# Performance work log

Measured on AMD Instinct MI355X. Metric: run time of the kernel, lower is better.

The kernel has to match this reference:

```python
import jax, jax.numpy as jnp
import numpy as np

D = 768
HEAD_DIM = 64
NHEADS = D // HEAD_DIM
B, S = 2, 4096


def setup_inputs() -> dict:
    key = jax.random.key(0)
    ks = jax.random.split(key, 9)
    std = 1.0 / np.sqrt(D)
    inp = {"x": jax.random.normal(ks[0], (B, S, D), dtype=jnp.float32)}
    for i, name in enumerate(["Wq", "Wk", "Wv", "Wo"]):
        inp[name + "_w"] = jax.random.uniform(ks[1 + 2 * i], (D, D), dtype=jnp.float32, minval=-std, maxval=std)
        inp[name + "_b"] = jax.random.uniform(ks[2 + 2 * i], (D,), dtype=jnp.float32, minval=-std, maxval=std)
    return inp


def reference(x, Wq_w, Wq_b, Wk_w, Wk_b, Wv_w, Wv_b, Wo_w, Wo_b):
    b, s, d = x.shape
    # nn.Linear: y = x @ W.T + b
    q = x @ Wq_w.T + Wq_b
    k = x @ Wk_w.T + Wk_b
    v = x @ Wv_w.T + Wv_b
    # [B, H, S, hd]
    q = q.reshape(b, s, NHEADS, HEAD_DIM).transpose(0, 2, 1, 3)
    k = k.reshape(b, s, NHEADS, HEAD_DIM).transpose(0, 2, 1, 3)
    v = v.reshape(b, s, NHEADS, HEAD_DIM).transpose(0, 2, 1, 3)
    scale = jnp.sqrt(jnp.asarray(HEAD_DIM, dtype=q.dtype))
    logits = jnp.einsum('bhqd,bhkd->bhqk', q, k) / scale  # [B,H,S,S]
    causal_mask = jnp.triu(jnp.ones((s, s), dtype=bool), k=1)
    logits = jnp.where(causal_mask, -jnp.inf, logits)
    a = jax.nn.softmax(logits, axis=-1)
    preout = jnp.einsum('bhqk,bhkd->bhqd', a, v)
    preout = preout.transpose(0, 2, 1, 3).reshape(b, s, d)
    return preout @ Wo_w.T + Wo_b
```

## Files before the change

### kernel.cpp

```cpp
#include <hip/hip_runtime.h>

typedef unsigned short u16;
typedef unsigned int u32;
typedef __bf16 bf16_t;
typedef bf16_t bf16x8 __attribute__((ext_vector_type(8)));
typedef float f32x2 __attribute__((ext_vector_type(2)));
typedef float f32x4 __attribute__((ext_vector_type(4)));
typedef float f32x16 __attribute__((ext_vector_type(16)));

#define DM 768
#define HD 64
#define NH 12
#define NB 2
#define SEQ 4096
#define MR (NB * SEQ)

#define SCL2E_F (0.125f * 1.44269504088896340736f)

__device__ __forceinline__ u16 f2bf(float f) {
  union { float f; u32 u; } v;
  v.f = f;
  u32 r = v.u + 0x7FFFu + ((v.u >> 16) & 1u);
  return (u16)(r >> 16);
}

__device__ __forceinline__ u32 cvtpk(float a, float b) {
  u32 r;
  asm("v_cvt_pk_bf16_f32 %0, %1, %2" : "=v"(r) : "v"(a), "v"(b));
  return r;
}

__device__ __forceinline__ void pl32swap(u32& a, u32& b) {
  asm volatile("v_permlane32_swap_b32 %0, %1" : "+v"(a), "+v"(b));
}

__device__ __forceinline__ f32x2 pkadd(f32x2 a, f32x2 b) {
  f32x2 r;
  asm("v_pk_add_f32 %0, %1, %2" : "=v"(r) : "v"(a), "v"(b));
  return r;
}

__device__ __forceinline__ bf16x8 ldb8(const u16* p) {
  return *reinterpret_cast<const bf16x8*>(p);
}

__device__ __forceinline__ f32x4 mfma16(bf16x8 a, bf16x8 b, f32x4 c) {
  return __builtin_amdgcn_mfma_f32_16x16x32_bf16(a, b, c, 0, 0, 0);
}

__device__ __forceinline__ f32x16 mfma32(bf16x8 a, bf16x8 b, f32x16 c) {
  return __builtin_amdgcn_mfma_f32_32x32x16_bf16(a, b, c, 0, 0, 0);
}

#define GLDS16(g, l)                                              \
  __builtin_amdgcn_global_load_lds(                               \
      (const __attribute__((address_space(1))) void*)(g),         \
      (__attribute__((address_space(3))) void*)(l), 16, 0, 0)

__global__ __launch_bounds__(256) void cvt_kernel(const float* __restrict__ src,
                                                  u16* __restrict__ dst, int n8) {
  int i = blockIdx.x * 256 + threadIdx.x;
  if (i >= n8) return;
  const float4* s = reinterpret_cast<const float4*>(src) + (size_t)i * 2;
  float4 a = s[0], b = s[1];
  union { u16 u[8]; uint4 v; } o;
  o.u[0] = f2bf(a.x); o.u[1] = f2bf(a.y); o.u[2] = f2bf(a.z); o.u[3] = f2bf(a.w);
  o.u[4] = f2bf(b.x); o.u[5] = f2bf(b.y); o.u[6] = f2bf(b.z); o.u[7] = f2bf(b.w);
  reinterpret_cast<uint4*>(dst)[i] = o.v;
}

__global__ __launch_bounds__(256) void cvt_w_kernel(const float* __restrict__ w0,
                                                    const float* __restrict__ w1,
                                                    const float* __restrict__ w2,
                                                    const float* __restrict__ w3,
                                                    u16* __restrict__ dst) {
  const float* src = (blockIdx.y == 0) ? w0 : (blockIdx.y == 1) ? w1
                   : (blockIdx.y == 2) ? w2 : w3;
  u16* d = dst + (size_t)blockIdx.y * DM * DM;
  int i = blockIdx.x * 256 + threadIdx.x;
  const float4* s = reinterpret_cast<const float4*>(src) + (size_t)i * 2;
  float4 a = s[0], b = s[1];
  union { u16 u[8]; uint4 v; } o;
  o.u[0] = f2bf(a.x); o.u[1] = f2bf(a.y); o.u[2] = f2bf(a.z); o.u[3] = f2bf(a.w);
  o.u[4] = f2bf(b.x); o.u[5] = f2bf(b.y); o.u[6] = f2bf(b.z); o.u[7] = f2bf(b.w);
  reinterpret_cast<uint4*>(d)[i] = o.v;
}

__global__ __launch_bounds__(256) void gemm_qkv_kernel(
    const u16* __restrict__ A, const u16* __restrict__ Wall,
    const float* __restrict__ b0, const float* __restrict__ b1,
    const float* __restrict__ b2, u16* __restrict__ O) {
  __shared__ __align__(16) u16 As[128 * 32];
  __shared__ __align__(16) u16 Bs[128 * 32];

  const int tid = threadIdx.x;
  const int w = tid >> 6, lane = tid & 63;
  const int l16 = lane & 15, lg = lane >> 4;
  const int wm = w >> 1, wn = w & 1;

  const int m0 = blockIdx.x * 128;
  const int n0 = blockIdx.y * 128;
  const int z = blockIdx.z;

  const u16* W = Wall + (size_t)z * DM * DM;
  const float* bias = (z == 0) ? b0 : ((z == 1) ? b1 : b2);
  u16* oz = O + (size_t)z * MR * DM;
  const float qscale = (z == 0) ? SCL2E_F : 1.f;

  f32x4 acc[4][4];
#pragma unroll
  for (int i = 0; i < 4; ++i)
#pragma unroll
    for (int j = 0; j < 4; ++j) {
      acc[i][j][0] = 0.f; acc[i][j][1] = 0.f;
      acc[i][j][2] = 0.f; acc[i][j][3] = 0.f;
    }

  for (int k0 = 0; k0 < DM; k0 += 32) {
#pragma unroll
    for (int i = 0; i < 2; ++i) {
      const int c = (w * 2 + i) * 64 + lane;
      const int m = c >> 2, kc = c & 3;
      GLDS16(A + (size_t)(m0 + m) * DM + (k0 + kc * 8),
             As + (size_t)(w * 2 + i) * 512);
      GLDS16(W + (size_t)(n0 + m) * DM + (k0 + kc * 8),
             Bs + (size_t)(w * 2 + i) * 512);
    }
    __syncthreads();
    bf16x8 af[4], bfv[4];
#pragma unroll
    for (int i = 0; i < 4; ++i)
      af[i] = ldb8(As + (wm * 64 + i * 16 + l16) * 32 + lg * 8);
#pragma unroll
    for (int j = 0; j < 4; ++j)
      bfv[j] = ldb8(Bs + (wn * 64 + j * 16 + l16) * 32 + lg * 8);
#pragma unroll
    for (int i = 0; i < 4; ++i)
#pragma unroll
      for (int j = 0; j < 4; ++j)
        acc[i][j] = mfma16(af[i], bfv[j], acc[i][j]);
    __syncthreads();
  }

#pragma unroll
  for (int i = 0; i < 4; ++i) {
    const int gm = m0 + wm * 64 + i * 16 + lg * 4;
    const int bb = gm >> 12;
    const int ss = gm & (SEQ - 1);
#pragma unroll
    for (int j = 0; j < 4; ++j) {
      const int gn = n0 + wn * 64 + j * 16 + l16;
      const int hh = gn >> 6, dd = gn & (HD - 1);
      const float bv = bias[gn];
      if (z == 2) {
        union { u16 u[4]; uint2 v; } pk;
#pragma unroll
        for (int r = 0; r < 4; ++r) pk.u[r] = f2bf(acc[i][j][r] + bv);
        *reinterpret_cast<uint2*>(
            oz + ((size_t)(bb * NH + hh) * HD + dd) * SEQ + ss) = pk.v;
      } else {
        u16* op = oz + ((size_t)(bb * NH + hh) * SEQ + ss) * HD + dd;
#pragma unroll
        for (int r = 0; r < 4; ++r)
          op[(size_t)r * HD] = f2bf((acc[i][j][r] + bv) * qscale);
      }
    }
  }
}

__global__ __launch_bounds__(256) void gemm_out_kernel(
    const u16* __restrict__ A, const u16* __restrict__ W,
    const float* __restrict__ bias, float* __restrict__ Out) {
  __shared__ __align__(16) u16 As[128 * 32];
  __shared__ __align__(16) u16 Bs[128 * 32];

  const int tid = threadIdx.x;
  const int w = tid >> 6, lane = tid & 63;
  const int l16 = lane & 15, lg = lane >> 4;
  const int wm = w >> 1, wn = w & 1;

  const int m0 = blockIdx.x * 128;
  const int n0 = blockIdx.y * 128;

  f32x4 acc[4][4];
#pragma unroll
  for (int i = 0; i < 4; ++i)
#pragma unroll
    for (int j = 0; j < 4; ++j) {
      acc[i][j][0] = 0.f; acc[i][j][1] = 0.f;
      acc[i][j][2] = 0.f; acc[i][j][3] = 0.f;
    }

  for (int k0 = 0; k0 < DM; k0 += 32) {
#pragma unroll
    for (int i = 0; i < 2; ++i) {
      const int c = (w * 2 + i) * 64 + lane;
      const int m = c >> 2, kc = c & 3;
      GLDS16(A + (size_t)(m0 + m) * DM + (k0 + kc * 8),
             As + (size_t)(w * 2 + i) * 512);
      GLDS16(W + (size_t)(n0 + m) * DM + (k0 + kc * 8),
             Bs + (size_t)(w * 2 + i) * 512);
    }
    __syncthreads();
    bf16x8 af[4], bfv[4];
#pragma unroll
    for (int i = 0; i < 4; ++i)
      af[i] = ldb8(As + (wm * 64 + i * 16 + l16) * 32 + lg * 8);
#pragma unroll
    for (int j = 0; j < 4; ++j)
      bfv[j] = ldb8(Bs + (wn * 64 + j * 16 + l16) * 32 + lg * 8);
#pragma unroll
    for (int i = 0; i < 4; ++i)
#pragma unroll
      for (int j = 0; j < 4; ++j)
        acc[i][j] = mfma16(af[i], bfv[j], acc[i][j]);
    __syncthreads();
  }

#pragma unroll
  for (int i = 0; i < 4; ++i) {
    const int gm = m0 + wm * 64 + i * 16 + lg * 4;
#pragma unroll
    for (int j = 0; j < 4; ++j) {
      const int gn = n0 + wn * 64 + j * 16 + l16;
      const float bv = bias[gn];
      float* op = Out + (size_t)gm * DM + gn;
#pragma unroll
      for (int r = 0; r < 4; ++r)
        op[(size_t)r * DM] = acc[i][j][r] + bv;
    }
  }
}

__global__ __launch_bounds__(256) void attn_kernel(
    const u16* __restrict__ Qg, const u16* __restrict__ Kg,
    const u16* __restrict__ VTg, u16* __restrict__ Og) {
  __shared__ __align__(16) u16 Kt[2][64][72];
  __shared__ __align__(16) u16 Vt[2][64][72];

  const int tid = threadIdx.x;
  const int w = tid >> 6, lane = tid & 63;
  const int l32 = lane & 31, hi = lane >> 5;

  const int idx = blockIdx.x;
  const int qt = 31 - (idx / 24);
  const int bh = idx % 24;
  const int bb = bh / NH, hh = bh % NH;

  const u16* Qp = Qg + (size_t)bh * SEQ * HD;
  const u16* Kp = Kg + (size_t)bh * SEQ * HD;
  const u16* VTp = VTg + (size_t)bh * HD * SEQ;

  const int qw0 = qt * 128 + w * 32;
  const int qlane = qw0 + l32;

  bf16x8 qf[4];
#pragma unroll
  for (int c = 0; c < 4; ++c)
    qf[c] = ldb8(Qp + (size_t)qlane * HD + c * 16 + hi * 8);

  f32x16 oacc[2];
#pragma unroll
  for (int db = 0; db < 2; ++db)
#pragma unroll
    for (int r = 0; r < 16; ++r) oacc[db][r] = 0.f;
  float lsum = 0.f;

  const int srow = tid >> 3;
  const int sc8 = (tid & 7) * 8;

  {
    uint4 a = *reinterpret_cast<const uint4*>(Kp + (size_t)srow * HD + sc8);
    uint4 b = *reinterpret_cast<const uint4*>(
        Kp + (size_t)(srow + 32) * HD + sc8);
    uint4 c = *reinterpret_cast<const uint4*>(
        VTp + (size_t)srow * SEQ + sc8);
    uint4 d = *reinterpret_cast<const uint4*>(
        VTp + (size_t)(srow + 32) * SEQ + sc8);
    *reinterpret_cast<uint4*>(&Kt[0][srow][sc8]) = a;
    *reinterpret_cast<uint4*>(&Kt[0][srow + 32][sc8]) = b;
    *reinterpret_cast<uint4*>(&Vt[0][srow][sc8]) = c;
    *reinterpret_cast<uint4*>(&Vt[0][srow + 32][sc8]) = d;
  }

  const int NT = 2 * qt + 2;
  int cur = 0;
  for (int t = 0; t < NT; ++t) {
    const int kv0 = t * 64;
    const bool pf = (t + 1 < NT);
    uint4 nK0, nK1, nV0, nV1;
    if (pf) {
      const int nk = kv0 + 64;
      nK0 = *reinterpret_cast<const uint4*>(
          Kp + (size_t)(nk + srow) * HD + sc8);
      nK1 = *reinterpret_cast<const uint4*>(
          Kp + (size_t)(nk + srow + 32) * HD + sc8);
      nV0 = *reinterpret_cast<const uint4*>(
          VTp + (size_t)srow * SEQ + nk + sc8);
      nV1 = *reinterpret_cast<const uint4*>(
          VTp + (size_t)(srow + 32) * SEQ + nk + sc8);
    }
    __syncthreads();

    const bool active = (kv0 <= qw0 + 31);
    f32x16 st[2];
    if (active) {
      __builtin_amdgcn_s_setprio(1);
#pragma unroll
      for (int b = 0; b < 2; ++b) {
#pragma unroll
        for (int r = 0; r < 16; ++r) st[b][r] = 0.f;
#pragma unroll
        for (int c = 0; c < 4; ++c) {
          bf16x8 kf = ldb8(&Kt[cur][b * 32 + l32][c * 16 + hi * 8]);
          st[b] = mfma32(kf, qf[c], st[b]);
        }
      }
      __builtin_amdgcn_s_setprio(0);

      if (kv0 + 63 > qw0) {
#pragma unroll
        for (int b = 0; b < 2; ++b)
#pragma unroll
          for (int r = 0; r < 16; ++r) {
            const int kvi = kv0 + b * 32 + (r & 3) + 8 * (r >> 2) + 4 * hi;
            if (kvi > qlane) st[b][r] = -__builtin_inff();
          }
      }

#pragma unroll
      for (int r = 0; r < 16; ++r) {
        st[0][r] = exp2f(st[0][r]);
        st[1][r] = exp2f(st[1][r]);
      }
      {
        const f32x2* h0 = reinterpret_cast<const f32x2*>(&st[0]);
        const f32x2* h1 = reinterpret_cast<const f32x2*>(&st[1]);
        f32x2 t2[8];
#pragma unroll
        for (int i = 0; i < 8; ++i) t2[i] = pkadd(h0[i], h1[i]);
#pragma unroll
        for (int i = 0; i < 4; ++i) t2[i] = pkadd(t2[i], t2[i + 4]);
        t2[0] = pkadd(t2[0], t2[2]);
        t2[1] = pkadd(t2[1], t2[3]);
        t2[0] = pkadd(t2[0], t2[1]);
        lsum += t2[0][0] + t2[0][1];
      }
    }

    if (pf) {
      *reinterpret_cast<uint4*>(&Kt[cur ^ 1][srow][sc8]) = nK0;
      *reinterpret_cast<uint4*>(&Kt[cur ^ 1][srow + 32][sc8]) = nK1;
      *reinterpret_cast<uint4*>(&Vt[cur ^ 1][srow][sc8]) = nV0;
      *reinterpret_cast<uint4*>(&Vt[cur ^ 1][srow + 32][sc8]) = nV1;
    }

    if (active) {
#pragma unroll
      for (int b = 0; b < 2; ++b) {
#pragma unroll
        for (int h = 0; h < 2; ++h) {
          u32 a0 = cvtpk(st[b][h * 8 + 0], st[b][h * 8 + 1]);
          u32 a1 = cvtpk(st[b][h * 8 + 2], st[b][h * 8 + 3]);
          u32 a2 = cvtpk(st[b][h * 8 + 4], st[b][h * 8 + 5]);
          u32 a3 = cvtpk(st[b][h * 8 + 6], st[b][h * 8 + 7]);
          pl32swap(a0, a2);
          pl32swap(a1, a3);
          union { u32 w[4]; bf16x8 v; } pb;
          pb.w[0] = a0; pb.w[1] = a1; pb.w[2] = a2; pb.w[3] = a3;
          const int c = 2 * b + h;
          __builtin_amdgcn_s_setprio(1);
#pragma unroll
          for (int db = 0; db < 2; ++db) {
            bf16x8 vf = ldb8(&Vt[cur][db * 32 + l32][c * 16 + hi * 8]);
            oacc[db] = mfma32(vf, pb.v, oacc[db]);
          }
          __builtin_amdgcn_s_setprio(0);
        }
      }
    }
    cur ^= 1;
  }

  const float ltot = lsum + __shfl_xor(lsum, 32);
  const float linv = 1.f / ltot;

  u16* Op = Og + ((size_t)bb * SEQ + qlane) * DM + hh * HD;
#pragma unroll
  for (int db = 0; db < 2; ++db)
#pragma unroll
    for (int r = 0; r < 16; r += 2) {
      const int d = db * 32 + (r & 3) + 8 * (r >> 2) + 4 * hi;
      u32 pk = cvtpk(oacc[db][r] * linv, oacc[db][r + 1] * linv);
      *reinterpret_cast<u32*>(Op + d) = pk;
    }
}

extern "C" void kernel_launch(void* const* d_in, const int* in_sizes, int n_in,
                              void* d_out, int out_size, void* d_ws,
                              size_t ws_size, hipStream_t stream) {
  const float* x  = (const float*)d_in[0];
  const float* Wq = (const float*)d_in[1];
  const float* bq = (const float*)d_in[2];
  const float* Wk = (const float*)d_in[3];
  const float* bk = (const float*)d_in[4];
  const float* Wv = (const float*)d_in[5];
  const float* bv = (const float*)d_in[6];
  const float* Wo = (const float*)d_in[7];
  const float* bo = (const float*)d_in[8];
  float* out = (float*)d_out;

  u16* xb   = (u16*)d_ws;
  u16* Wall = xb + (size_t)MR * DM;
  u16* QKV  = Wall + (size_t)4 * DM * DM;
  u16* PRE  = QKV + (size_t)3 * MR * DM;

  cvt_kernel<<<dim3(MR * DM / 8 / 256), 256, 0, stream>>>(x, xb, MR * DM / 8);
  cvt_w_kernel<<<dim3(DM * DM / 8 / 256, 4), 256, 0, stream>>>(Wq, Wk, Wv, Wo,
                                                               Wall);
  gemm_qkv_kernel<<<dim3(MR / 128, DM / 128, 3), 256, 0, stream>>>(
      xb, Wall, bq, bk, bv, QKV);
  attn_kernel<<<dim3(768), 256, 0, stream>>>(
      QKV, QKV + (size_t)MR * DM, QKV + (size_t)2 * MR * DM, PRE);
  gemm_out_kernel<<<dim3(MR / 128, DM / 128), 256, 0, stream>>>(
      PRE, Wall + (size_t)3 * DM * DM, bo, out);
}
```

Baseline: 189.8 us.

## Split long causal query tiles across two blocks with atomic partial combine

Query tiles in the upper half of the sequence have their KV range split into two halves, each run by its own block. The blocks are ordered with a custom rank mapping to balance work across the grid. Split blocks atomically add unnormalized fp32 partial outputs and row sums into zeroed workspace buffers, and a new combine kernel normalizes them and writes bf16. This aims to cut the tail imbalance of causal attention, at the cost of two memsets, atomic traffic and an extra kernel launch. It relies on softmax without a running max, which makes the partial results additive.

Measured after the change: 312.6 us. 64.7% more time.

```diff
diff --git a/kernel.cpp b/kernel.cpp
--- a/kernel.cpp
+++ b/kernel.cpp
@@ -234,7 +234,8 @@
 
 __global__ __launch_bounds__(256) void attn_kernel(
     const u16* __restrict__ Qg, const u16* __restrict__ Kg,
-    const u16* __restrict__ VTg, u16* __restrict__ Og) {
+    const u16* __restrict__ VTg, u16* __restrict__ Og,
+    float* __restrict__ PO, float* __restrict__ PL) {
   __shared__ __align__(16) u16 Kt[2][64][72];
   __shared__ __align__(16) u16 Vt[2][64][72];
 
@@ -243,8 +244,27 @@
   const int l32 = lane & 31, hi = lane >> 5;
 
   const int idx = blockIdx.x;
-  const int qt = 31 - (idx / 24);
+  const int rank = idx / 24;
   const int bh = idx % 24;
+  int j;
+  if (rank < 40) {
+    const int g = rank / 5, r5 = rank % 5;
+    j = (r5 == 0) ? (15 - g)
+                  : ((r5 < 3) ? (46 - 4 * g + (r5 - 1))
+                              : (44 - 4 * g + (r5 - 3)));
+  } else {
+    j = 47 - rank;
+  }
+  int qt, t0, t1;
+  bool direct;
+  if (j < 16) {
+    qt = j; t0 = 0; t1 = 2 * j + 2; direct = true;
+  } else {
+    const int s = j - 16;
+    qt = 16 + (s >> 1);
+    const int L = qt + 1;
+    t0 = (s & 1) * L; t1 = t0 + L; direct = false;
+  }
   const int bb = bh / NH, hh = bh % NH;
 
   const u16* Qp = Qg + (size_t)bh * SEQ * HD;
@@ -270,24 +290,25 @@
   const int sc8 = (tid & 7) * 8;
 
   {
-    uint4 a = *reinterpret_cast<const uint4*>(Kp + (size_t)srow * HD + sc8);
+    const int kb = t0 * 64;
+    uint4 a = *reinterpret_cast<const uint4*>(
+        Kp + (size_t)(kb + srow) * HD + sc8);
     uint4 b = *reinterpret_cast<const uint4*>(
-        Kp + (size_t)(srow + 32) * HD + sc8);
+        Kp + (size_t)(kb + srow + 32) * HD + sc8);
     uint4 c = *reinterpret_cast<const uint4*>(
-        VTp + (size_t)srow * SEQ + sc8);
+        VTp + (size_t)srow * SEQ + kb + sc8);
     uint4 d = *reinterpret_cast<const uint4*>(
-        VTp + (size_t)(srow + 32) * SEQ + sc8);
+        VTp + (size_t)(srow + 32) * SEQ + kb + sc8);
     *reinterpret_cast<uint4*>(&Kt[0][srow][sc8]) = a;
     *reinterpret_cast<uint4*>(&Kt[0][srow + 32][sc8]) = b;
     *reinterpret_cast<uint4*>(&Vt[0][srow][sc8]) = c;
     *reinterpret_cast<uint4*>(&Vt[0][srow + 32][sc8]) = d;
   }
 
-  const int NT = 2 * qt + 2;
   int cur = 0;
-  for (int t = 0; t < NT; ++t) {
+  for (int t = t0; t < t1; ++t) {
     const int kv0 = t * 64;
-    const bool pf = (t + 1 < NT);
+    const bool pf = (t + 1 < t1);
     uint4 nK0, nK1, nV0, nV1;
     if (pf) {
       const int nk = kv0 + 64;
@@ -383,17 +404,54 @@
   }
 
   const float ltot = lsum + __shfl_xor(lsum, 32);
-  const float linv = 1.f / ltot;
-
-  u16* Op = Og + ((size_t)bb * SEQ + qlane) * DM + hh * HD;
-#pragma unroll
-  for (int db = 0; db < 2; ++db)
-#pragma unroll
-    for (int r = 0; r < 16; r += 2) {
-      const int d = db * 32 + (r & 3) + 8 * (r >> 2) + 4 * hi;
-      u32 pk = cvtpk(oacc[db][r] * linv, oacc[db][r + 1] * linv);
-      *reinterpret_cast<u32*>(Op + d) = pk;
-    }
+
+  if (direct) {
+    const float linv = 1.f / ltot;
+    u16* Op = Og + ((size_t)bb * SEQ + qlane) * DM + hh * HD;
+#pragma unroll
+    for (int db = 0; db < 2; ++db)
+#pragma unroll
+      for (int r = 0; r < 16; r += 2) {
+        const int d = db * 32 + (r & 3) + 8 * (r >> 2) + 4 * hi;
+        u32 pk = cvtpk(oacc[db][r] * linv, oacc[db][r + 1] * linv);
+        *reinterpret_cast<u32*>(Op + d) = pk;
+      }
+  } else {
+    const int grp = bh * 16 + (qt - 16);
+    const int qrow = w * 32 + l32;
+    float* pbase = PO + ((size_t)grp * 128 + qrow) * 64;
+#pragma unroll
+    for (int db = 0; db < 2; ++db)
+#pragma unroll
+      for (int r = 0; r < 16; ++r) {
+        const int d = db * 32 + (r & 3) + 8 * (r >> 2) + 4 * hi;
+        unsafeAtomicAdd(pbase + d, oacc[db][r]);
+      }
+    if (hi == 0) unsafeAtomicAdd(PL + grp * 128 + qrow, ltot);
+  }
+}
+
+__global__ __launch_bounds__(256) void combine_kernel(
+    const float* __restrict__ PO, const float* __restrict__ PL,
+    u16* __restrict__ Og) {
+  const int blk = blockIdx.x;
+  const int bh = blk % 24, qt16 = blk / 24;
+  const int bb = bh / NH, hh = bh % NH;
+  const int tid = threadIdx.x;
+  const int q = tid >> 1;
+  const int d0 = (tid & 1) * 32;
+  const int grp = bh * 16 + qt16;
+  const float* po = PO + ((size_t)grp * 128 + q) * 64 + d0;
+  const float linv = 1.f / PL[grp * 128 + q];
+  const int srow = (16 + qt16) * 128 + q;
+  u16* op = Og + ((size_t)bb * SEQ + srow) * DM + hh * HD + d0;
+  u32 pk[16];
+#pragma unroll
+  for (int i = 0; i < 16; ++i)
+    pk[i] = cvtpk(po[2 * i] * linv, po[2 * i + 1] * linv);
+#pragma unroll
+  for (int i = 0; i < 4; ++i)
+    reinterpret_cast<uint4*>(op)[i] = *reinterpret_cast<const uint4*>(&pk[4 * i]);
 }
 
 extern "C" void kernel_launch(void* const* d_in, const int* in_sizes, int n_in,
@@ -414,14 +472,19 @@
   u16* Wall = xb + (size_t)MR * DM;
   u16* QKV  = Wall + (size_t)4 * DM * DM;
   u16* PRE  = QKV + (size_t)3 * MR * DM;
+  float* PO = (float*)d_ws;
+  float* PL = (float*)(PRE + (size_t)MR * DM);
 
   cvt_kernel<<<dim3(MR * DM / 8 / 256), 256, 0, stream>>>(x, xb, MR * DM / 8);
   cvt_w_kernel<<<dim3(DM * DM / 8 / 256, 4), 256, 0, stream>>>(Wq, Wk, Wv, Wo,
                                                                Wall);
   gemm_qkv_kernel<<<dim3(MR / 128, DM / 128, 3), 256, 0, stream>>>(
       xb, Wall, bq, bk, bv, QKV);
-  attn_kernel<<<dim3(768), 256, 0, stream>>>(
-      QKV, QKV + (size_t)MR * DM, QKV + (size_t)2 * MR * DM, PRE);
+  hipMemsetAsync(PO, 0, (size_t)384 * 128 * 64 * 4, stream);
+  hipMemsetAsync(PL, 0, (size_t)384 * 128 * 4, stream);
+  attn_kernel<<<dim3(1152), 256, 0, stream>>>(
+      QKV, QKV + (size_t)MR * DM, QKV + (size_t)2 * MR * DM, PRE, PO, PL);
+  combine_kernel<<<dim3(384), 256, 0, stream>>>(PO, PL, PRE);
   gemm_out_kernel<<<dim3(MR / 128, DM / 128), 256, 0, stream>>>(
       PRE, Wall + (size_t)3 * DM * DM, bo, out);
 }
```
